# Kernel tuning notes

Hardware: AMD Instinct MI355X
Metric: run time of the kernel (lower is better)

The kernel has to match this reference:

```python
import jax, jax.numpy as jnp
import numpy as np

EPS = 1e-10
NUM_NODES = 100000
OUT_CH = 128
NUM_EDGES = 600000


def setup_inputs() -> dict:
    key = jax.random.key(0)
    k1, k2, k3, k4, k5, k6 = jax.random.split(key, 6)
    emb = jax.random.normal(k1, (NUM_NODES, OUT_CH), dtype=jnp.float32) * 0.02
    edge_index = jax.random.randint(k2, (2, NUM_EDGES), 0, NUM_NODES, dtype=jnp.int32)
    edge_norm = jax.random.uniform(k3, (NUM_EDGES,), dtype=jnp.float32)
    lim = 1.0 / np.sqrt(OUT_CH)
    loc_w = jax.random.uniform(k4, (OUT_CH, OUT_CH), minval=-lim, maxval=lim, dtype=jnp.float32)
    loc_b = jnp.zeros((OUT_CH,), dtype=jnp.float32)
    std_w = jax.random.uniform(k5, (OUT_CH, OUT_CH), minval=-lim, maxval=lim, dtype=jnp.float32)
    std_b = jnp.zeros((OUT_CH,), dtype=jnp.float32)
    return {"emb": emb, "loc_w": loc_w, "loc_b": loc_b, "std_w": std_w,
            "std_b": std_b, "edge_index": edge_index, "edge_norm": edge_norm}


def reference(emb, loc_w, loc_b, std_w, std_b, edge_index, edge_norm):
    sidx, tidx = edge_index[0], edge_index[1]
    # gather-scale-scatter graph conv: message[e] = emb[sidx[e]] * enorm[e]
    message = emb[sidx] * edge_norm[:, None]          # [E, C]
    ptr = jax.ops.segment_sum(message, tidx, num_segments=emb.shape[0])  # [N, C]
    loc = ptr @ loc_w.T + loc_b                        # [N, C]
    std = jax.nn.softplus(ptr @ std_w.T + std_b) + EPS # [N, C]
    # eval mode: emb_out = loc (dist is Normal(loc, std), returned as params)
    return (loc, std)
```

## Files before the change

### kernel.cpp

```cpp
#include <hip/hip_runtime.h>
#include <hip/hip_bf16.h>
#include <stdint.h>

#define OUT_CH 128
#define EPSV 1e-10f

typedef __attribute__((ext_vector_type(4))) float f32x4;
typedef __attribute__((ext_vector_type(8))) short bf16x8;

__device__ __forceinline__ ushort f2bf(float f) {
    union { float f; unsigned u; } a; a.f = f;
    unsigned u = a.u;
    unsigned r = (u + 0x7fffu + ((u >> 16) & 1u)) >> 16;
    return (ushort)r;
}

__global__ __launch_bounds__(256) void hist_convert_kernel(
    const int* __restrict__ eidx, int* __restrict__ cnt, int E, int HB,
    const float* __restrict__ locw, const float* __restrict__ stdw,
    int4* __restrict__ Wb)
{
    int b = blockIdx.x;
    if (b < HB) {
        int e = b * 256 + threadIdx.x;
        if (e < E) atomicAdd(&cnt[eidx[E + e]], 1);
    } else {
        int q = (b - HB) * 256 + threadIdx.x;
        int r = q >> 4;
        int c = q & 15;
        const float* src = (r < 128) ? (locw + r * 128 + c * 8)
                                     : (stdw + (r - 128) * 128 + c * 8);
        float4 u0 = *reinterpret_cast<const float4*>(src);
        float4 u1 = *reinterpret_cast<const float4*>(src + 4);
        unsigned p0 = (unsigned)f2bf(u0.x) | ((unsigned)f2bf(u0.y) << 16);
        unsigned p1 = (unsigned)f2bf(u0.z) | ((unsigned)f2bf(u0.w) << 16);
        unsigned p2 = (unsigned)f2bf(u1.x) | ((unsigned)f2bf(u1.y) << 16);
        unsigned p3 = (unsigned)f2bf(u1.z) | ((unsigned)f2bf(u1.w) << 16);
        Wb[q] = make_int4((int)p0, (int)p1, (int)p2, (int)p3);
    }
}

__device__ __forceinline__ int block_exscan256(int v, int* lds, int* totalOut) {
    int t = threadIdx.x;
    lds[t] = v; __syncthreads();
    #pragma unroll
    for (int d = 1; d < 256; d <<= 1) {
        int x = (t >= d) ? lds[t - d] : 0;
        __syncthreads();
        lds[t] += x;
        __syncthreads();
    }
    int inc = lds[t];
    int tot = lds[255];
    __syncthreads();
    *totalOut = tot;
    return inc - v;
}

__global__ __launch_bounds__(256) void block_sum_kernel(
    const int* __restrict__ cnt, int* __restrict__ bsum, int N)
{
    __shared__ int lds[256];
    int base = blockIdx.x * 1024;
    int local = 0;
    #pragma unroll
    for (int k = 0; k < 4; ++k) {
        int idx = base + threadIdx.x * 4 + k;
        local += (idx < N) ? cnt[idx] : 0;
    }
    lds[threadIdx.x] = local; __syncthreads();
    for (int d = 128; d > 0; d >>= 1) {
        if (threadIdx.x < d) lds[threadIdx.x] += lds[threadIdx.x + d];
        __syncthreads();
    }
    if (threadIdx.x == 0) bsum[blockIdx.x] = lds[0];
}

__global__ __launch_bounds__(256) void top_scan_kernel(
    const int* __restrict__ bsum, int* __restrict__ bofs, int NB)
{
    __shared__ int lds[256];
    int t = threadIdx.x;
    int v = (t < NB) ? bsum[t] : 0;
    int total;
    int ex = block_exscan256(v, lds, &total);
    if (t < NB) bofs[t] = ex;
}

__global__ __launch_bounds__(256) void scan_final_kernel(
    const int* __restrict__ cnt, const int* __restrict__ bofs,
    int* __restrict__ cursor, int N)
{
    __shared__ int lds[256];
    int base = blockIdx.x * 1024;
    int c[4]; int local = 0;
    #pragma unroll
    for (int k = 0; k < 4; ++k) {
        int idx = base + threadIdx.x * 4 + k;
        c[k] = (idx < N) ? cnt[idx] : 0;
        local += c[k];
    }
    int total;
    int ex = block_exscan256(local, lds, &total);
    int run = bofs[blockIdx.x] + ex;
    #pragma unroll
    for (int k = 0; k < 4; ++k) {
        int idx = base + threadIdx.x * 4 + k;
        if (idx < N) { cursor[idx] = run; run += c[k]; }
    }
}

__global__ __launch_bounds__(256) void fill_kernel(
    const int* __restrict__ eidx, const float* __restrict__ enorm,
    int* __restrict__ cursor, int2* __restrict__ srcw, int E)
{
    int e = blockIdx.x * 256 + threadIdx.x;
    if (e >= E) return;
    int t = eidx[E + e];
    int s = eidx[e];
    float w = enorm[e];
    int pos = atomicAdd(&cursor[t], 1);
    srcw[pos] = make_int2(s, __float_as_int(w));
}

__global__ __launch_bounds__(256) void gather_kernel(
    const float* __restrict__ emb, const int* __restrict__ cursor,
    const int* __restrict__ cnt, const int2* __restrict__ srcw,
    unsigned* __restrict__ ptrb, int N)
{
    int wid = (blockIdx.x * 256 + threadIdx.x) >> 6;
    if (wid >= N) return;
    int lane = threadIdx.x & 63;
    int c = cnt[wid];
    int o = cursor[wid] - c;
    const float2* emb2 = (const float2*)emb;
    float ax = 0.f, ay = 0.f;
    int j = 0;
    for (; j + 4 <= c; j += 4) {
        int2 p0 = srcw[o + j + 0];
        int2 p1 = srcw[o + j + 1];
        int2 p2 = srcw[o + j + 2];
        int2 p3 = srcw[o + j + 3];
        float2 v0 = emb2[(size_t)p0.x * 64 + lane];
        float2 v1 = emb2[(size_t)p1.x * 64 + lane];
        float2 v2 = emb2[(size_t)p2.x * 64 + lane];
        float2 v3 = emb2[(size_t)p3.x * 64 + lane];
        float w0 = __int_as_float(p0.y), w1 = __int_as_float(p1.y);
        float w2 = __int_as_float(p2.y), w3 = __int_as_float(p3.y);
        ax += v0.x * w0 + v1.x * w1 + v2.x * w2 + v3.x * w3;
        ay += v0.y * w0 + v1.y * w1 + v2.y * w2 + v3.y * w3;
    }
    for (; j < c; ++j) {
        int2 p = srcw[o + j];
        float w = __int_as_float(p.y);
        float2 v = emb2[(size_t)p.x * 64 + lane];
        ax += v.x * w;
        ay += v.y * w;
    }
    ptrb[(size_t)wid * 128 + lane] = (unsigned)f2bf(ax) | ((unsigned)f2bf(ay) << 16);
}

__global__ __launch_bounds__(256, 2) void gemm_kernel(
    const int4* __restrict__ Wb, const float* __restrict__ locb,
    const float* __restrict__ stdb, float* __restrict__ out, int N)
{
    __shared__ ushort Wt[256 * 128];
    const int t = threadIdx.x;

    #pragma unroll
    for (int i = 0; i < 16; ++i) {
        int q = i * 256 + t;
        int r = q >> 4;
        int c = q & 15;
        int4 v = Wb[q];
        *reinterpret_cast<int4*>(&Wt[r * 128 + ((c ^ (r & 15)) << 3)]) = v;
    }
    __syncthreads();

    const int wave = t >> 6;
    const int lane = t & 63;
    const int grp = lane >> 4;
    const int l16 = lane & 15;
    const int base = blockIdx.x * 128 + wave * 32;

    const ushort* ptrb = (const ushort*)out;
    int r0 = base + l16;      if (r0 > N - 1) r0 = N - 1;
    int r1 = base + 16 + l16; if (r1 > N - 1) r1 = N - 1;

    bf16x8 a0[4], a1[4];
    #pragma unroll
    for (int s = 0; s < 4; ++s) {
        a0[s] = *reinterpret_cast<const bf16x8*>(ptrb + (size_t)r0 * 256 + s * 32 + grp * 8);
        a1[s] = *reinterpret_cast<const bf16x8*>(ptrb + (size_t)r1 * 256 + s * 32 + grp * 8);
    }

    f32x4 acc0[16], acc1[16];
    #pragma unroll
    for (int j = 0; j < 16; ++j) {
        acc0[j] = (f32x4){0.f, 0.f, 0.f, 0.f};
        acc1[j] = (f32x4){0.f, 0.f, 0.f, 0.f};
    }

    #pragma unroll
    for (int j = 0; j < 16; ++j) {
        int cb = (j * 16 + l16) * 128;
        #pragma unroll
        for (int s = 0; s < 4; ++s) {
            int c = s * 4 + grp;
            bf16x8 bfr = *reinterpret_cast<const bf16x8*>(&Wt[cb + ((c ^ l16) << 3)]);
            acc0[j] = __builtin_amdgcn_mfma_f32_16x16x32_bf16(a0[s], bfr, acc0[j], 0, 0, 0);
            acc1[j] = __builtin_amdgcn_mfma_f32_16x16x32_bf16(a1[s], bfr, acc1[j], 0, 0, 0);
        }
    }

    #pragma unroll
    for (int j = 0; j < 16; ++j) {
        int col = j * 16 + l16;
        bool isStd = col >= 128;
        int wcol = col & 127;
        float bias = isStd ? stdb[wcol] : locb[wcol];
        float* dst = isStd ? (out + (size_t)N * OUT_CH) : out;
        #pragma unroll
        for (int tile = 0; tile < 2; ++tile) {
            #pragma unroll
            for (int rg = 0; rg < 4; ++rg) {
                int node = base + tile * 16 + grp * 4 + rg;
                if (node < N) {
                    float x = (tile ? acc1[j][rg] : acc0[j][rg]) + bias;
                    if (isStd) x = __logf(1.0f + __expf(x)) + EPSV;
                    dst[(size_t)node * OUT_CH + wcol] = x;
                }
            }
        }
    }
}

extern "C" void kernel_launch(void* const* d_in, const int* in_sizes, int n_in,
                              void* d_out, int out_size, void* d_ws, size_t ws_size,
                              hipStream_t stream) {
    const float* emb  = (const float*)d_in[0];
    const float* locw = (const float*)d_in[1];
    const float* locb = (const float*)d_in[2];
    const float* stdw = (const float*)d_in[3];
    const float* stdb = (const float*)d_in[4];
    const int*   eidx = (const int*)d_in[5];
    const float* enorm= (const float*)d_in[6];
    float* out = (float*)d_out;

    const int N = in_sizes[0] / OUT_CH;
    const int E = in_sizes[6];
    const int NB = (N + 1023) / 1024;
    const int HB = (E + 255) / 256;

    int* cnt    = (int*)d_ws;
    int* cursor = cnt + N;
    int* bsum   = cursor + N;
    int* bofs   = bsum + 256;
    int2* srcw  = (int2*)(((uintptr_t)(bofs + 256) + 255) & ~(uintptr_t)255);
    int4* Wb    = (int4*)(((uintptr_t)(srcw + E) + 255) & ~(uintptr_t)255);

    hipMemsetAsync(cnt, 0, (size_t)N * sizeof(int), stream);

    hist_convert_kernel<<<HB + 16, 256, 0, stream>>>(eidx, cnt, E, HB, locw, stdw, Wb);
    block_sum_kernel<<<NB, 256, 0, stream>>>(cnt, bsum, N);
    top_scan_kernel<<<1, 256, 0, stream>>>(bsum, bofs, NB);
    scan_final_kernel<<<NB, 256, 0, stream>>>(cnt, bofs, cursor, N);
    fill_kernel<<<(E + 255) / 256, 256, 0, stream>>>(eidx, enorm, cursor, srcw, E);

    unsigned* ptrb = (unsigned*)out;
    long gthreads = (long)N * 64;
    gather_kernel<<<(int)((gthreads + 255) / 256), 256, 0, stream>>>(emb, cursor, cnt, srcw, ptrb, N);

    int nblocks = (N + 127) / 128;
    gemm_kernel<<<nblocks, 256, 0, stream>>>(Wb, locb, stdb, out, N);
}
```

Before: 310.7 us.

## Pre-convert embeddings to bf16 for gather and split GEMM into two halves

Adds a pass inside the histogram kernel that converts the fp32 embedding table to bf16, staged in the std half of the output buffer. The gather kernel then reads 4-byte packed bf16 pairs instead of 8-byte float2, halving the bytes moved by its random row reads. In exchange it pays a streaming convert pass over the table and rounds the inputs to bf16 earlier, which adds some error. Separately, the GEMM now loads loc and std weights one half at a time into a smaller LDS buffer and raises the occupancy hint from 2 to 4 blocks, at the cost of an extra barrier and weight reload per block.

After: 293.0 us. 5.7% less time.

```diff
diff --git a/kernel.cpp b/kernel.cpp
--- a/kernel.cpp
+++ b/kernel.cpp
@@ -16,15 +16,15 @@
 }
 
 __global__ __launch_bounds__(256) void hist_convert_kernel(
-    const int* __restrict__ eidx, int* __restrict__ cnt, int E, int HB,
+    const int* __restrict__ eidx, int* __restrict__ cnt, int E, int HB, int EB,
     const float* __restrict__ locw, const float* __restrict__ stdw,
-    int4* __restrict__ Wb)
+    int4* __restrict__ Wb, const float* __restrict__ emb, int4* __restrict__ embb4)
 {
     int b = blockIdx.x;
     if (b < HB) {
         int e = b * 256 + threadIdx.x;
         if (e < E) atomicAdd(&cnt[eidx[E + e]], 1);
-    } else {
+    } else if (b < HB + 16) {
         int q = (b - HB) * 256 + threadIdx.x;
         int r = q >> 4;
         int c = q & 15;
@@ -37,6 +37,16 @@
         unsigned p2 = (unsigned)f2bf(u1.x) | ((unsigned)f2bf(u1.y) << 16);
         unsigned p3 = (unsigned)f2bf(u1.z) | ((unsigned)f2bf(u1.w) << 16);
         Wb[q] = make_int4((int)p0, (int)p1, (int)p2, (int)p3);
+    } else {
+        int idx8 = (b - HB - 16) * 256 + threadIdx.x;
+        const float4* e4 = (const float4*)emb;
+        float4 u0 = e4[(size_t)idx8 * 2];
+        float4 u1 = e4[(size_t)idx8 * 2 + 1];
+        unsigned p0 = (unsigned)f2bf(u0.x) | ((unsigned)f2bf(u0.y) << 16);
+        unsigned p1 = (unsigned)f2bf(u0.z) | ((unsigned)f2bf(u0.w) << 16);
+        unsigned p2 = (unsigned)f2bf(u1.x) | ((unsigned)f2bf(u1.y) << 16);
+        unsigned p3 = (unsigned)f2bf(u1.z) | ((unsigned)f2bf(u1.w) << 16);
+        embb4[idx8] = make_int4((int)p0, (int)p1, (int)p2, (int)p3);
     }
 }
 
@@ -124,7 +134,7 @@
 }
 
 __global__ __launch_bounds__(256) void gather_kernel(
-    const float* __restrict__ emb, const int* __restrict__ cursor,
+    const unsigned* __restrict__ embb, const int* __restrict__ cursor,
     const int* __restrict__ cnt, const int2* __restrict__ srcw,
     unsigned* __restrict__ ptrb, int N)
 {
@@ -133,7 +143,6 @@
     int lane = threadIdx.x & 63;
     int c = cnt[wid];
     int o = cursor[wid] - c;
-    const float2* emb2 = (const float2*)emb;
     float ax = 0.f, ay = 0.f;
     int j = 0;
     for (; j + 4 <= c; j += 4) {
@@ -141,42 +150,33 @@
         int2 p1 = srcw[o + j + 1];
         int2 p2 = srcw[o + j + 2];
         int2 p3 = srcw[o + j + 3];
-        float2 v0 = emb2[(size_t)p0.x * 64 + lane];
-        float2 v1 = emb2[(size_t)p1.x * 64 + lane];
-        float2 v2 = emb2[(size_t)p2.x * 64 + lane];
-        float2 v3 = emb2[(size_t)p3.x * 64 + lane];
+        unsigned v0 = embb[(size_t)p0.x * 64 + lane];
+        unsigned v1 = embb[(size_t)p1.x * 64 + lane];
+        unsigned v2 = embb[(size_t)p2.x * 64 + lane];
+        unsigned v3 = embb[(size_t)p3.x * 64 + lane];
         float w0 = __int_as_float(p0.y), w1 = __int_as_float(p1.y);
         float w2 = __int_as_float(p2.y), w3 = __int_as_float(p3.y);
-        ax += v0.x * w0 + v1.x * w1 + v2.x * w2 + v3.x * w3;
-        ay += v0.y * w0 + v1.y * w1 + v2.y * w2 + v3.y * w3;
+        ax += __uint_as_float(v0 << 16) * w0 + __uint_as_float(v1 << 16) * w1
+            + __uint_as_float(v2 << 16) * w2 + __uint_as_float(v3 << 16) * w3;
+        ay += __uint_as_float(v0 & 0xffff0000u) * w0 + __uint_as_float(v1 & 0xffff0000u) * w1
+            + __uint_as_float(v2 & 0xffff0000u) * w2 + __uint_as_float(v3 & 0xffff0000u) * w3;
     }
     for (; j < c; ++j) {
         int2 p = srcw[o + j];
         float w = __int_as_float(p.y);
-        float2 v = emb2[(size_t)p.x * 64 + lane];
-        ax += v.x * w;
-        ay += v.y * w;
+        unsigned v = embb[(size_t)p.x * 64 + lane];
+        ax += __uint_as_float(v << 16) * w;
+        ay += __uint_as_float(v & 0xffff0000u) * w;
     }
     ptrb[(size_t)wid * 128 + lane] = (unsigned)f2bf(ax) | ((unsigned)f2bf(ay) << 16);
 }
 
-__global__ __launch_bounds__(256, 2) void gemm_kernel(
+__global__ __launch_bounds__(256, 4) void gemm_kernel(
     const int4* __restrict__ Wb, const float* __restrict__ locb,
     const float* __restrict__ stdb, float* __restrict__ out, int N)
 {
-    __shared__ ushort Wt[256 * 128];
+    __shared__ ushort Wt[128 * 128];
     const int t = threadIdx.x;
-
-    #pragma unroll
-    for (int i = 0; i < 16; ++i) {
-        int q = i * 256 + t;
-        int r = q >> 4;
-        int c = q & 15;
-        int4 v = Wb[q];
-        *reinterpret_cast<int4*>(&Wt[r * 128 + ((c ^ (r & 15)) << 3)]) = v;
-    }
-    __syncthreads();
-
     const int wave = t >> 6;
     const int lane = t & 63;
     const int grp = lane >> 4;
@@ -194,41 +194,53 @@
         a1[s] = *reinterpret_cast<const bf16x8*>(ptrb + (size_t)r1 * 256 + s * 32 + grp * 8);
     }
 
-    f32x4 acc0[16], acc1[16];
-    #pragma unroll
-    for (int j = 0; j < 16; ++j) {
-        acc0[j] = (f32x4){0.f, 0.f, 0.f, 0.f};
-        acc1[j] = (f32x4){0.f, 0.f, 0.f, 0.f};
-    }
-
-    #pragma unroll
-    for (int j = 0; j < 16; ++j) {
-        int cb = (j * 16 + l16) * 128;
-        #pragma unroll
-        for (int s = 0; s < 4; ++s) {
-            int c = s * 4 + grp;
-            bf16x8 bfr = *reinterpret_cast<const bf16x8*>(&Wt[cb + ((c ^ l16) << 3)]);
-            acc0[j] = __builtin_amdgcn_mfma_f32_16x16x32_bf16(a0[s], bfr, acc0[j], 0, 0, 0);
-            acc1[j] = __builtin_amdgcn_mfma_f32_16x16x32_bf16(a1[s], bfr, acc1[j], 0, 0, 0);
-        }
-    }
-
-    #pragma unroll
-    for (int j = 0; j < 16; ++j) {
-        int col = j * 16 + l16;
-        bool isStd = col >= 128;
-        int wcol = col & 127;
-        float bias = isStd ? stdb[wcol] : locb[wcol];
-        float* dst = isStd ? (out + (size_t)N * OUT_CH) : out;
-        #pragma unroll
-        for (int tile = 0; tile < 2; ++tile) {
+    #pragma unroll
+    for (int h = 0; h < 2; ++h) {
+        if (h) __syncthreads();
+        #pragma unroll
+        for (int i = 0; i < 8; ++i) {
+            int q = i * 256 + t;
+            int r = q >> 4;
+            int c = q & 15;
+            *reinterpret_cast<int4*>(&Wt[r * 128 + ((c ^ (r & 15)) << 3)]) =
+                Wb[(h * 128 + r) * 16 + c];
+        }
+        __syncthreads();
+
+        f32x4 acc0[8], acc1[8];
+        #pragma unroll
+        for (int j = 0; j < 8; ++j) {
+            acc0[j] = (f32x4){0.f, 0.f, 0.f, 0.f};
+            acc1[j] = (f32x4){0.f, 0.f, 0.f, 0.f};
+        }
+
+        #pragma unroll
+        for (int j = 0; j < 8; ++j) {
+            int cb = (j * 16 + l16) * 128;
             #pragma unroll
-            for (int rg = 0; rg < 4; ++rg) {
-                int node = base + tile * 16 + grp * 4 + rg;
-                if (node < N) {
-                    float x = (tile ? acc1[j][rg] : acc0[j][rg]) + bias;
-                    if (isStd) x = __logf(1.0f + __expf(x)) + EPSV;
-                    dst[(size_t)node * OUT_CH + wcol] = x;
+            for (int s = 0; s < 4; ++s) {
+                int c = s * 4 + grp;
+                bf16x8 bfr = *reinterpret_cast<const bf16x8*>(&Wt[cb + ((c ^ l16) << 3)]);
+                acc0[j] = __builtin_amdgcn_mfma_f32_16x16x32_bf16(a0[s], bfr, acc0[j], 0, 0, 0);
+                acc1[j] = __builtin_amdgcn_mfma_f32_16x16x32_bf16(a1[s], bfr, acc1[j], 0, 0, 0);
+            }
+        }
+
+        float* dst = h ? (out + (size_t)N * OUT_CH) : out;
+        #pragma unroll
+        for (int j = 0; j < 8; ++j) {
+            int col = j * 16 + l16;
+            float bias = h ? stdb[col] : locb[col];
+            #pragma unroll
+            for (int tile = 0; tile < 2; ++tile) {
+                #pragma unroll
+                for (int rg = 0; rg < 4; ++rg) {
+                    int node = base + tile * 16 + grp * 4 + rg;
+                    if (node < N) {
+                        float x = (tile ? acc1[j][rg] : acc0[j][rg]) + bias;
+                        if (h) x = __logf(1.0f + __expf(x)) + EPSV;
+                        dst[(size_t)node * OUT_CH + col] = x;
+                    }
                 }
             }
         }
@@ -251,6 +263,7 @@
     const int E = in_sizes[6];
     const int NB = (N + 1023) / 1024;
     const int HB = (E + 255) / 256;
+    const int EB = (N * (OUT_CH / 8) + 255) / 256;
 
     int* cnt    = (int*)d_ws;
     int* cursor = cnt + N;
@@ -259,9 +272,12 @@
     int2* srcw  = (int2*)(((uintptr_t)(bofs + 256) + 255) & ~(uintptr_t)255);
     int4* Wb    = (int4*)(((uintptr_t)(srcw + E) + 255) & ~(uintptr_t)255);
 
+    unsigned* embb = (unsigned*)(out + (size_t)N * OUT_CH);
+
     hipMemsetAsync(cnt, 0, (size_t)N * sizeof(int), stream);
 
-    hist_convert_kernel<<<HB + 16, 256, 0, stream>>>(eidx, cnt, E, HB, locw, stdw, Wb);
+    hist_convert_kernel<<<HB + 16 + EB, 256, 0, stream>>>(
+        eidx, cnt, E, HB, EB, locw, stdw, Wb, emb, (int4*)embb);
     block_sum_kernel<<<NB, 256, 0, stream>>>(cnt, bsum, N);
     top_scan_kernel<<<1, 256, 0, stream>>>(bsum, bofs, NB);
     scan_final_kernel<<<NB, 256, 0, stream>>>(cnt, bofs, cursor, N);
@@ -269,7 +285,7 @@
 
     unsigned* ptrb = (unsigned*)out;
     long gthreads = (long)N * 64;
-    gather_kernel<<<(int)((gthreads + 255) / 256), 256, 0, stream>>>(emb, cursor, cnt, srcw, ptrb, N);
+    gather_kernel<<<(int)((gthreads + 255) / 256), 256, 0, stream>>>(embb, cursor, cnt, srcw, ptrb, N);
 
     int nblocks = (N + 127) / 128;
     gemm_kernel<<<nblocks, 256, 0, stream>>>(Wb, locb, stdb, out, N);
```
